# Kernel tuning notes

Measured on AMD Instinct MI355X. Metric: run time of the kernel, lower is better.

Reference implementation:

```python
import jax, jax.numpy as jnp
import numpy as np

HEADS = 16
D_MODEL = 1024
D_HEAD = D_MODEL // HEADS


def setup_inputs() -> dict:
    key = jax.random.key(0)
    ks = jax.random.split(key, 12)
    B, S = 4, 2048
    scale = D_MODEL ** -0.5
    inp = {
        "q": jax.random.normal(ks[0], (B, S, D_MODEL), jnp.float32),
        "k": jax.random.normal(ks[1], (B, S, D_MODEL), jnp.float32),
        "v": jax.random.normal(ks[2], (B, S, D_MODEL), jnp.float32),
        # causal mask: True = masked position
        "mask": jnp.triu(jnp.ones((S, S), bool), k=1)[None].repeat(B, axis=0),
        "wq": jax.random.normal(ks[3], (D_MODEL, D_MODEL), jnp.float32) * scale,
        "bq": jnp.zeros((D_MODEL,), jnp.float32),
        "wk": jax.random.normal(ks[4], (D_MODEL, D_MODEL), jnp.float32) * scale,
        "bk": jnp.zeros((D_MODEL,), jnp.float32),
        "wv": jax.random.normal(ks[5], (D_MODEL, D_MODEL), jnp.float32) * scale,
        "bv": jnp.zeros((D_MODEL,), jnp.float32),
        "wo": jax.random.normal(ks[6], (D_MODEL, D_MODEL), jnp.float32) * scale,
        "bo": jnp.zeros((D_MODEL,), jnp.float32),
    }
    return inp


def _split_head(x):
    B, S, _ = x.shape
    return x.reshape(B, S, HEADS, D_HEAD).transpose(0, 2, 1, 3)  # [B,H,S,D]


def reference(q, k, v, mask, wq, bq, wk, bk, wv, bv, wo, bo):
    # linear projections (torch Linear: x @ W^T + b)
    qh = _split_head(q @ wq.T + bq) * (D_HEAD ** -0.5)
    kh = _split_head(k @ wk.T + bk)
    vh = _split_head(v @ wv.T + bv)
    # scores [B,H,Sq,Sk]
    scores = jnp.einsum("bhqd,bhkd->bhqk", qh, kh)
    scores = jnp.where(mask[:, None, :, :], -1e20, scores)
    weights = jax.nn.softmax(scores, axis=-1)  # dropout p=0 in eval
    ctx = jnp.einsum("bhqk,bhkd->bhqd", weights, vh)
    B, H, S, D = ctx.shape
    ctx = ctx.transpose(0, 2, 1, 3).reshape(B, S, H * D)
    return ctx @ wo.T + bo
```

## Files before the change

### kernel.cpp

```cpp
#include <hip/hip_runtime.h>
#include <hip/hip_bf16.h>
#include <cstdint>
#include <cstddef>

typedef unsigned short u16;
typedef unsigned int u32;
using short8  = __attribute__((ext_vector_type(8))) short;
using f32x4   = __attribute__((ext_vector_type(4))) float;
using f32x16  = __attribute__((ext_vector_type(16))) float;
using u32x4   = __attribute__((ext_vector_type(4))) u32;

#define SCALE_Q 0.18033688011112043f

#define WAITVM(N) asm volatile("s_waitcnt vmcnt(" #N ")" ::: "memory")

__device__ inline u16 f2bf(float f) {
  return __builtin_bit_cast(u16, __float2bfloat16(f));
}

__device__ inline u32 cvt_pk_bf16(float a, float b) {
  u32 r;
  asm("v_cvt_pk_bf16_f32 %0, %1, %2" : "=v"(r) : "v"(a), "v"(b));
  return r;
}

__device__ inline f32x4 mfma16(short8 a, short8 b, f32x4 c) {
  return __builtin_amdgcn_mfma_f32_16x16x32_bf16(a, b, c, 0, 0, 0);
}
__device__ inline f32x16 mfma32(short8 a, short8 b, f32x16 c) {
  return __builtin_amdgcn_mfma_f32_32x32x16_bf16(a, b, c, 0, 0, 0);
}

__device__ inline void gload16(const void* g, void* l) {
  __builtin_amdgcn_global_load_lds(
      (const __attribute__((address_space(1))) void*)g,
      (__attribute__((address_space(3))) void*)l,
      16, 0, 0);
}

__global__ __launch_bounds__(256)
void prep(const float* __restrict__ q, const float* __restrict__ k,
          const float* __restrict__ v,
          const float* __restrict__ wq, const float* __restrict__ wk,
          const float* __restrict__ wv, const float* __restrict__ wo,
          u16* __restrict__ Wb, u16* __restrict__ Act) {
  const int c = blockIdx.x * 256 + threadIdx.x;
  const float* src;
  u16* dst;
  float sc = 1.f;
  size_t off;
  if (c < 524288) {
    const int m = c >> 17;
    off = (size_t)(c & 131071) * 8;
    src = (m == 0) ? wq : (m == 1) ? wk : (m == 2) ? wv : wo;
    if (m == 0) sc = SCALE_Q;
    dst = Wb + (size_t)m * 1048576;
  } else {
    const int c2 = c - 524288;
    const int m = c2 >> 20;
    off = (size_t)(c2 & 1048575) * 8;
    src = (m == 0) ? q : (m == 1) ? k : v;
    dst = Act + (size_t)m * 8388608;
  }
  f32x4 a = *(const f32x4*)(src + off);
  f32x4 b = *(const f32x4*)(src + off + 4);
  short8 vv;
#pragma unroll
  for (int j = 0; j < 4; ++j) { vv[j] = (short)f2bf(a[j] * sc); vv[4 + j] = (short)f2bf(b[j] * sc); }
  *(short8*)&dst[off] = vv;
}

struct GemmArgs {
  const u16* Act; const u16* ctx; const u16* Wb;
  const float* bq; const float* bk; const float* bv; const float* bo;
  u16* Qs; u16* Ks; u16* Vs; float* out;
};

__global__ __launch_bounds__(256, 3)
void gemm_proj(GemmArgs ga, int modeBase) {
  const int mode = modeBase + blockIdx.z;
  const int bx = blockIdx.x;
  const int bm = ((bx & 7) << 3) | (bx >> 3);
  const int bn = blockIdx.y;
  const int tid = threadIdx.x;
  const int w = tid >> 6, lane = tid & 63;
  const int wr = w >> 1, wc = w & 1;
  const int l15 = lane & 15, g = lane >> 4;

  const u16* Am = (mode == 3) ? ga.ctx : ga.Act + (size_t)mode * 8388608;
  const u16* Wm = ga.Wb + (size_t)mode * 1048576;
  const float* bias = (mode == 0) ? ga.bq : (mode == 1) ? ga.bk : (mode == 2) ? ga.bv : ga.bo;

  __shared__ u16 As[2][128 * 64];
  __shared__ u16 Bs[2][128 * 64];

  f32x4 acc[4][4] = {};
  const int m0 = bm * 128, n0 = bn * 128;

  const int r_lo = lane >> 3;
  const int sc8 = ((lane & 7) ^ (lane >> 3)) * 8;

  auto stage = [&](int k0, int slot) {
#pragma unroll
    for (int i = 0; i < 4; ++i) {
      const int row = i * 32 + w * 8 + r_lo;
      const int db = i * 2048 + w * 512;
      gload16(Am + (size_t)(m0 + row) * 1024 + k0 + sc8, &As[slot][db]);
      gload16(Wm + (size_t)(n0 + row) * 1024 + k0 + sc8, &Bs[slot][db]);
    }
  };

  auto compute = [&](int slot) {
#pragma unroll
    for (int kk = 0; kk < 2; ++kk) {
      short8 av[4], bv4[4];
#pragma unroll
      for (int mi = 0; mi < 4; ++mi) {
        const int row = wr * 64 + mi * 16 + l15;
        av[mi] = *(const short8*)&As[slot][row * 64 + ((((kk << 2) | g)) ^ (row & 7)) * 8];
      }
#pragma unroll
      for (int ni = 0; ni < 4; ++ni) {
        const int row = wc * 64 + ni * 16 + l15;
        bv4[ni] = *(const short8*)&Bs[slot][row * 64 + ((((kk << 2) | g)) ^ (row & 7)) * 8];
      }
#pragma unroll
      for (int mi = 0; mi < 4; ++mi)
#pragma unroll
        for (int ni = 0; ni < 4; ++ni)
          acc[mi][ni] = mfma16(av[mi], bv4[ni], acc[mi][ni]);
    }
  };

  stage(0, 0);
  stage(64, 1);

#pragma unroll 2
  for (int t = 0; t < 14; ++t) {
    WAITVM(8);
    __builtin_amdgcn_s_barrier();
    __builtin_amdgcn_sched_barrier(0);
    compute(t & 1);
    __builtin_amdgcn_s_barrier();
    __builtin_amdgcn_sched_barrier(0);
    stage((t + 2) * 64, t & 1);
  }
  WAITVM(8);
  __builtin_amdgcn_s_barrier();
  __builtin_amdgcn_sched_barrier(0);
  compute(0);
  WAITVM(0);
  __builtin_amdgcn_s_barrier();
  __builtin_amdgcn_sched_barrier(0);
  compute(1);

  float bvals[4];
#pragma unroll
  for (int ni = 0; ni < 4; ++ni)
    bvals[ni] = bias[n0 + wc * 64 + ni * 16 + l15] * ((mode == 0) ? SCALE_Q : 1.f);

  if (mode == 3) {
#pragma unroll
    for (int mi = 0; mi < 4; ++mi)
#pragma unroll
      for (int ni = 0; ni < 4; ++ni)
#pragma unroll
        for (int r = 0; r < 4; ++r) {
          const int m = m0 + wr * 64 + mi * 16 + g * 4 + r;
          const int n = n0 + wc * 64 + ni * 16 + l15;
          ga.out[(size_t)m * 1024 + n] = acc[mi][ni][r] + bvals[ni];
        }
  } else {
    u16* O = (mode == 0) ? ga.Qs : (mode == 1) ? ga.Ks : ga.Vs;
#pragma unroll
    for (int mi = 0; mi < 4; ++mi)
#pragma unroll
      for (int ni = 0; ni < 4; ++ni)
#pragma unroll
        for (int r = 0; r < 4; ++r) {
          const int m = m0 + wr * 64 + mi * 16 + g * 4 + r;
          const int n = n0 + wc * 64 + ni * 16 + l15;
          const int b = m >> 11, s = m & 2047, hh = n >> 6, d = n & 63;
          const float val = acc[mi][ni][r] + bvals[ni];
          const size_t base = (size_t)(b * 16 + hh) * 131072;
          size_t idx;
          if (mode == 2) {
            const int sp = (s & ~12) | ((s & 4) << 1) | ((s & 8) >> 1);
            const int kt = sp >> 5, w5 = sp & 31;
            const int j = ((d >> 5) << 1) | (w5 >> 4);
            const int hi2 = (w5 >> 3) & 1, e = w5 & 7;
            idx = base + (size_t)kt * 2048 + j * 512 + hi2 * 256 + (d & 31) * 8 + e;
          } else {
            const int s32 = s >> 5, l31 = s & 31;
            const int t2 = d >> 4, hi2 = (d >> 3) & 1, e = d & 7;
            idx = base + (size_t)s32 * 2048 + t2 * 512 + hi2 * 256 + l31 * 8 + e;
          }
          O[idx] = f2bf(val);
        }
  }
}

__global__ __launch_bounds__(256)
void attn_fwd(const u16* __restrict__ Qs, const u16* __restrict__ Ks,
              const u16* __restrict__ Vs, u16* __restrict__ ctx) {
  const int bh = blockIdx.x;
  const int qt = 15 - blockIdx.y;
  const int tid = threadIdx.x;
  const int w = tid >> 6, lane = tid & 63;
  const int l31 = lane & 31, hi = lane >> 5;

  const u16* Qb = Qs + (size_t)bh * 131072;
  const u16* Kb = Ks + (size_t)bh * 131072;
  const u16* Vb = Vs + (size_t)bh * 131072;
  const int b = bh >> 4, hh = bh & 15;

  const int qw0 = qt * 128 + w * 32;
  const int nktw = (qw0 >> 5) + 1;
  const int nktmax = qt * 4 + 4;
  const int qrow = qw0 + l31;

  __shared__ u16 Klds[2][2048];
  __shared__ u16 Vlds[2][2048];

  auto stageKV = [&](int kt, int slot) {
    const size_t toff = (size_t)kt * 2048 + (w * 64 + lane) * 8;
    gload16(Kb + toff, &Klds[slot][w * 512]);
    gload16(Vb + toff, &Vlds[slot][w * 512]);
  };

  stageKV(0, 0);
  stageKV(1, 1);
  __builtin_amdgcn_sched_barrier(0);

  short8 qf[4];
  {
    const u16* qp = Qb + (size_t)(qw0 >> 5) * 2048 + lane * 8;
#pragma unroll
    for (int t = 0; t < 4; ++t) qf[t] = *(const short8*)(qp + t * 512);
  }
  __builtin_amdgcn_sched_barrier(0);

  f32x16 oacc0 = {}, oacc1 = {};
  float lsum = 0.f;

  for (int kt = 0; kt < nktmax; ++kt) {
    const int slot = kt & 1;
    if (kt + 1 < nktmax) { WAITVM(2); } else { WAITVM(0); }
    __builtin_amdgcn_s_barrier();
    __builtin_amdgcn_sched_barrier(0);

    short8 kf[4], vf[4];
#pragma unroll
    for (int t = 0; t < 4; ++t) {
      kf[t] = *(const short8*)&Klds[slot][t * 512 + lane * 8];
      vf[t] = *(const short8*)&Vlds[slot][t * 512 + lane * 8];
    }

    f32x16 st = {};
    __builtin_amdgcn_s_setprio(1);
    st = mfma32(kf[0], qf[0], st);
    st = mfma32(kf[1], qf[1], st);
    st = mfma32(kf[2], qf[2], st);
    st = mfma32(kf[3], qf[3], st);
    __builtin_amdgcn_s_setprio(0);

    if (kt >= nktw - 1) {
#pragma unroll
      for (int r = 0; r < 16; ++r) {
        const int ka = kt * 32 + (r & 3) + 8 * (r >> 2) + 4 * hi;
        if (ka > qrow) st[r] = -1e30f;
      }
    }

    float p[16];
#pragma unroll
    for (int r = 0; r < 16; ++r) p[r] = __builtin_amdgcn_exp2f(st[r]);
    {
      float s0 = (p[0] + p[1]) + (p[2] + p[3]);
      float s1 = (p[4] + p[5]) + (p[6] + p[7]);
      float s2 = (p[8] + p[9]) + (p[10] + p[11]);
      float s3 = (p[12] + p[13]) + (p[14] + p[15]);
      lsum += (s0 + s1) + (s2 + s3);
    }
    u32x4 a0, a1;
#pragma unroll
    for (int v2 = 0; v2 < 4; ++v2) {
      a0[v2] = cvt_pk_bf16(p[2 * v2], p[2 * v2 + 1]);
      a1[v2] = cvt_pk_bf16(p[8 + 2 * v2], p[9 + 2 * v2]);
    }
    const short8 pb0 = __builtin_bit_cast(short8, a0);
    const short8 pb1 = __builtin_bit_cast(short8, a1);
    __builtin_amdgcn_s_setprio(1);
    oacc0 = mfma32(vf[0], pb0, oacc0);
    oacc0 = mfma32(vf[1], pb1, oacc0);
    oacc1 = mfma32(vf[2], pb0, oacc1);
    oacc1 = mfma32(vf[3], pb1, oacc1);
    __builtin_amdgcn_s_setprio(0);

    __builtin_amdgcn_s_barrier();
    __builtin_amdgcn_sched_barrier(0);
    if (kt + 2 < nktmax) stageKV(kt + 2, slot);
  }

  lsum += __shfl_xor(lsum, 32);
  const float inv = __builtin_amdgcn_rcpf(lsum);

  u16* crow = ctx + ((size_t)(b * 2048 + qrow)) * 1024 + hh * 64;
#pragma unroll
  for (int r = 0; r < 16; r += 2) {
    const int d0 = (r & 3) + 8 * (r >> 2) + 4 * hi;
    *(u32*)&crow[d0]      = cvt_pk_bf16(oacc0[r] * inv, oacc0[r + 1] * inv);
    *(u32*)&crow[32 + d0] = cvt_pk_bf16(oacc1[r] * inv, oacc1[r + 1] * inv);
  }
}

extern "C" void kernel_launch(void* const* d_in, const int* in_sizes, int n_in,
                              void* d_out, int out_size, void* d_ws, size_t ws_size,
                              hipStream_t stream) {
  const float* q  = (const float*)d_in[0];
  const float* k  = (const float*)d_in[1];
  const float* v  = (const float*)d_in[2];
  const float* wq = (const float*)d_in[4];
  const float* bq = (const float*)d_in[5];
  const float* wk = (const float*)d_in[6];
  const float* bk = (const float*)d_in[7];
  const float* wv = (const float*)d_in[8];
  const float* bv = (const float*)d_in[9];
  const float* wo = (const float*)d_in[10];
  const float* bo = (const float*)d_in[11];

  char* ws = (char*)d_ws;
  const size_t WBSZ  = (size_t)4 * 1048576 * sizeof(u16);
  const size_t ACTSZ = (size_t)3 * 8388608 * sizeof(u16);
  const size_t SZ    = (size_t)64 * 131072 * sizeof(u16);
  u16* Wb  = (u16*)(ws);
  u16* Act = (u16*)(ws + WBSZ);
  u16* Qs  = (u16*)(ws + WBSZ + ACTSZ);
  u16* Ks  = (u16*)(ws + WBSZ + ACTSZ + SZ);
  u16* Vs  = (u16*)(ws + WBSZ + ACTSZ + 2 * SZ);
  u16* ctx = (u16*)(ws + WBSZ + ACTSZ + 3 * SZ);

  GemmArgs ga;
  ga.Act = Act; ga.ctx = ctx; ga.Wb = Wb;
  ga.bq = bq; ga.bk = bk; ga.bv = bv; ga.bo = bo;
  ga.Qs = Qs; ga.Ks = Ks; ga.Vs = Vs; ga.out = (float*)d_out;

  prep<<<dim3(14336), dim3(256), 0, stream>>>(q, k, v, wq, wk, wv, wo, Wb, Act);
  gemm_proj<<<dim3(64, 8, 3), dim3(256), 0, stream>>>(ga, 0);
  attn_fwd<<<dim3(64, 16), dim3(256), 0, stream>>>(Qs, Ks, Vs, ctx);
  gemm_proj<<<dim3(64, 8, 1), dim3(256), 0, stream>>>(ga, 3);
}
```

Before: 176.9 us.

## Fuse fp32-to-bf16 activation conversion into QKV projection GEMM A-tile loads

The prep kernel no longer converts the q/k/v activations to bf16; it only converts the weights. The QKV projection GEMM, now a FUSED template instance, loads fp32 activation tiles into registers, packs them to bf16 with v_cvt_pk_bf16, and writes them to LDS in the same swizzled layout, using a register double buffer. This removes a full activation write and re-read through a bf16 workspace. In exchange, the GEMM reads twice as many A bytes per tile, routes them through VGPRs instead of direct-to-LDS loads, and adds explicit lgkm waits to the pipeline.

```diff
diff --git a/kernel.cpp b/kernel.cpp
--- a/kernel.cpp
+++ b/kernel.cpp
@@ -13,6 +13,7 @@
 #define SCALE_Q 0.18033688011112043f
 
 #define WAITVM(N) asm volatile("s_waitcnt vmcnt(" #N ")" ::: "memory")
+#define LGKM0    asm volatile("s_waitcnt lgkmcnt(0)" ::: "memory")
 
 __device__ inline u16 f2bf(float f) {
   return __builtin_bit_cast(u16, __float2bfloat16(f));
@@ -39,43 +40,30 @@
 }
 
 __global__ __launch_bounds__(256)
-void prep(const float* __restrict__ q, const float* __restrict__ k,
-          const float* __restrict__ v,
-          const float* __restrict__ wq, const float* __restrict__ wk,
+void prep(const float* __restrict__ wq, const float* __restrict__ wk,
           const float* __restrict__ wv, const float* __restrict__ wo,
-          u16* __restrict__ Wb, u16* __restrict__ Act) {
+          u16* __restrict__ Wb) {
   const int c = blockIdx.x * 256 + threadIdx.x;
-  const float* src;
-  u16* dst;
-  float sc = 1.f;
-  size_t off;
-  if (c < 524288) {
-    const int m = c >> 17;
-    off = (size_t)(c & 131071) * 8;
-    src = (m == 0) ? wq : (m == 1) ? wk : (m == 2) ? wv : wo;
-    if (m == 0) sc = SCALE_Q;
-    dst = Wb + (size_t)m * 1048576;
-  } else {
-    const int c2 = c - 524288;
-    const int m = c2 >> 20;
-    off = (size_t)(c2 & 1048575) * 8;
-    src = (m == 0) ? q : (m == 1) ? k : v;
-    dst = Act + (size_t)m * 8388608;
-  }
+  const int m = c >> 17;
+  const size_t off = (size_t)(c & 131071) * 8;
+  const float* src = (m == 0) ? wq : (m == 1) ? wk : (m == 2) ? wv : wo;
+  const float sc = (m == 0) ? SCALE_Q : 1.f;
   f32x4 a = *(const f32x4*)(src + off);
   f32x4 b = *(const f32x4*)(src + off + 4);
   short8 vv;
 #pragma unroll
   for (int j = 0; j < 4; ++j) { vv[j] = (short)f2bf(a[j] * sc); vv[4 + j] = (short)f2bf(b[j] * sc); }
-  *(short8*)&dst[off] = vv;
+  *(short8*)&Wb[(size_t)m * 1048576 + off] = vv;
 }
 
 struct GemmArgs {
-  const u16* Act; const u16* ctx; const u16* Wb;
+  const float* qf; const float* kf; const float* vf;
+  const u16* ctx; const u16* Wb;
   const float* bq; const float* bk; const float* bv; const float* bo;
   u16* Qs; u16* Ks; u16* Vs; float* out;
 };
 
+template<bool FUSED>
 __global__ __launch_bounds__(256, 3)
 void gemm_proj(GemmArgs ga, int modeBase) {
   const int mode = modeBase + blockIdx.z;
@@ -87,8 +75,9 @@
   const int wr = w >> 1, wc = w & 1;
   const int l15 = lane & 15, g = lane >> 4;
 
-  const u16* Am = (mode == 3) ? ga.ctx : ga.Act + (size_t)mode * 8388608;
-  const u16* Wm = ga.Wb + (size_t)mode * 1048576;
+  const float* Af = (mode == 0) ? ga.qf : (mode == 1) ? ga.kf : ga.vf;
+  const u16*   Am = ga.ctx;
+  const u16*   Wm = ga.Wb + (size_t)mode * 1048576;
   const float* bias = (mode == 0) ? ga.bq : (mode == 1) ? ga.bk : (mode == 2) ? ga.bv : ga.bo;
 
   __shared__ u16 As[2][128 * 64];
@@ -98,15 +87,38 @@
   const int m0 = bm * 128, n0 = bn * 128;
 
   const int r_lo = lane >> 3;
-  const int sc8 = ((lane & 7) ^ (lane >> 3)) * 8;
-
-  auto stage = [&](int k0, int slot) {
+  const int sclog = (lane & 7) ^ (lane >> 3);
+  const int sc8 = sclog * 8;
+
+  auto stageB = [&](int k0, int slot) {
+#pragma unroll
+    for (int i = 0; i < 4; ++i)
+      gload16(Wm + (size_t)(n0 + i * 32 + w * 8 + r_lo) * 1024 + k0 + sc8,
+              &Bs[slot][i * 2048 + w * 512]);
+  };
+  auto stageA_lds = [&](int k0, int slot) {
+#pragma unroll
+    for (int i = 0; i < 4; ++i)
+      gload16(Am + (size_t)(m0 + i * 32 + w * 8 + r_lo) * 1024 + k0 + sc8,
+              &As[slot][i * 2048 + w * 512]);
+  };
+  auto loadA = [&](int k0, f32x4 (&r)[8]) {
 #pragma unroll
     for (int i = 0; i < 4; ++i) {
-      const int row = i * 32 + w * 8 + r_lo;
-      const int db = i * 2048 + w * 512;
-      gload16(Am + (size_t)(m0 + row) * 1024 + k0 + sc8, &As[slot][db]);
-      gload16(Wm + (size_t)(n0 + row) * 1024 + k0 + sc8, &Bs[slot][db]);
+      const float* src = Af + (size_t)(m0 + i * 32 + w * 8 + r_lo) * 1024 + k0 + sc8;
+      r[2 * i]     = *(const f32x4*)(src);
+      r[2 * i + 1] = *(const f32x4*)(src + 4);
+    }
+  };
+  auto writeA = [&](f32x4 (&r)[8], int slot) {
+#pragma unroll
+    for (int i = 0; i < 4; ++i) {
+      u32x4 wv;
+      wv[0] = cvt_pk_bf16(r[2 * i][0], r[2 * i][1]);
+      wv[1] = cvt_pk_bf16(r[2 * i][2], r[2 * i][3]);
+      wv[2] = cvt_pk_bf16(r[2 * i + 1][0], r[2 * i + 1][1]);
+      wv[3] = cvt_pk_bf16(r[2 * i + 1][2], r[2 * i + 1][3]);
+      *(u32x4*)&As[slot][i * 2048 + w * 512 + lane * 8] = wv;
     }
   };
 
@@ -132,27 +144,66 @@
     }
   };
 
-  stage(0, 0);
-  stage(64, 1);
-
+  if (FUSED) {
+    f32x4 rA[8], rB[8];
+    stageB(0, 0);  loadA(0, rA);
+    stageB(64, 1); loadA(64, rB);
+    WAITVM(12);
+    writeA(rA, 0);
+    LGKM0;
+    for (int tt = 0; tt < 14; tt += 2) {
+      __builtin_amdgcn_s_barrier();
+      __builtin_amdgcn_sched_barrier(0);
+      compute(0);
+      __builtin_amdgcn_s_barrier();
+      __builtin_amdgcn_sched_barrier(0);
+      stageB((tt + 2) * 64, 0); loadA((tt + 2) * 64, rA);
+      WAITVM(12);
+      writeA(rB, 1);
+      LGKM0;
+      __builtin_amdgcn_s_barrier();
+      __builtin_amdgcn_sched_barrier(0);
+      compute(1);
+      __builtin_amdgcn_s_barrier();
+      __builtin_amdgcn_sched_barrier(0);
+      stageB((tt + 3) * 64, 1); loadA((tt + 3) * 64, rB);
+      WAITVM(12);
+      writeA(rA, 0);
+      LGKM0;
+    }
+    __builtin_amdgcn_s_barrier();
+    __builtin_amdgcn_sched_barrier(0);
+    compute(0);
+    __builtin_amdgcn_s_barrier();
+    __builtin_amdgcn_sched_barrier(0);
+    WAITVM(0);
+    writeA(rB, 1);
+    LGKM0;
+    __builtin_amdgcn_s_barrier();
+    __builtin_amdgcn_sched_barrier(0);
+    compute(1);
+  } else {
+    stageA_lds(0, 0);  stageB(0, 0);
+    stageA_lds(64, 1); stageB(64, 1);
 #pragma unroll 2
-  for (int t = 0; t < 14; ++t) {
+    for (int t = 0; t < 14; ++t) {
+      WAITVM(8);
+      __builtin_amdgcn_s_barrier();
+      __builtin_amdgcn_sched_barrier(0);
+      compute(t & 1);
+      __builtin_amdgcn_s_barrier();
+      __builtin_amdgcn_sched_barrier(0);
+      stageA_lds((t + 2) * 64, t & 1); stageB((t + 2) * 64, t & 1);
+    }
     WAITVM(8);
     __builtin_amdgcn_s_barrier();
     __builtin_amdgcn_sched_barrier(0);
-    compute(t & 1);
-    __builtin_amdgcn_s_barrier();
-    __builtin_amdgcn_sched_barrier(0);
-    stage((t + 2) * 64, t & 1);
+    compute(0);
+    WAITVM(0);
+    __builtin_amdgcn_s_barrier();
+    __builtin_amdgcn_sched_barrier(0);
+    compute(1);
   }
-  WAITVM(8);
-  __builtin_amdgcn_s_barrier();
-  __builtin_amdgcn_sched_barrier(0);
-  compute(0);
-  WAITVM(0);
-  __builtin_amdgcn_s_barrier();
-  __builtin_amdgcn_sched_barrier(0);
-  compute(1);
 
   float bvals[4];
 #pragma unroll
@@ -330,23 +381,21 @@
   const float* bo = (const float*)d_in[11];
 
   char* ws = (char*)d_ws;
-  const size_t WBSZ  = (size_t)4 * 1048576 * sizeof(u16);
-  const size_t ACTSZ = (size_t)3 * 8388608 * sizeof(u16);
-  const size_t SZ    = (size_t)64 * 131072 * sizeof(u16);
+  const size_t WBSZ = (size_t)4 * 1048576 * sizeof(u16);
+  const size_t SZ   = (size_t)64 * 131072 * sizeof(u16);
   u16* Wb  = (u16*)(ws);
-  u16* Act = (u16*)(ws + WBSZ);
-  u16* Qs  = (u16*)(ws + WBSZ + ACTSZ);
-  u16* Ks  = (u16*)(ws + WBSZ + ACTSZ + SZ);
-  u16* Vs  = (u16*)(ws + WBSZ + ACTSZ + 2 * SZ);
-  u16* ctx = (u16*)(ws + WBSZ + ACTSZ + 3 * SZ);
+  u16* Qs  = (u16*)(ws + WBSZ);
+  u16* Ks  = (u16*)(ws + WBSZ + SZ);
+  u16* Vs  = (u16*)(ws + WBSZ + 2 * SZ);
+  u16* ctx = (u16*)(ws + WBSZ + 3 * SZ);
 
   GemmArgs ga;
-  ga.Act = Act; ga.ctx = ctx; ga.Wb = Wb;
+  ga.qf = q; ga.kf = k; ga.vf = v; ga.ctx = ctx; ga.Wb = Wb;
   ga.bq = bq; ga.bk = bk; ga.bv = bv; ga.bo = bo;
   ga.Qs = Qs; ga.Ks = Ks; ga.Vs = Vs; ga.out = (float*)d_out;
 
-  prep<<<dim3(14336), dim3(256), 0, stream>>>(q, k, v, wq, wk, wv, wo, Wb, Act);
-  gemm_proj<<<dim3(64, 8, 3), dim3(256), 0, stream>>>(ga, 0);
+  prep<<<dim3(2048), dim3(256), 0, stream>>>(wq, wk, wv, wo, Wb);
+  gemm_proj<true><<<dim3(64, 8, 3), dim3(256), 0, stream>>>(ga, 0);
   attn_fwd<<<dim3(64, 16), dim3(256), 0, stream>>>(Qs, Ks, Vs, ctx);
-  gemm_proj<<<dim3(64, 8, 1), dim3(256), 0, stream>>>(ga, 3);
-}
+  gemm_proj<false><<<dim3(64, 8, 1), dim3(256), 0, stream>>>(ga, 3);
+}
```

Result: faster. 170.0 us (-3.9%).
